# Kernel tuning notes

Measured on AMD Instinct MI355X. Metric: run time of the kernel, lower is better.

The kernel has to match this reference:

```python
import jax, jax.numpy as jnp
import numpy as np

# Topologies derived from init kwargs (inputs=64, outputs=64, state=512, net1 hidden=[512])
D = 64 + 64 + 512                      # 640 = concat(input, prev_output, state)
NET1 = [D, 512, 64]
NET3 = [D] + NET1 + [512]              # [640, 640, 512, 64, 512] (code reuses mutated net1 topo)
W_TOTAL = sum(NET3[j] * NET3[j + 1] for j in range(len(NET3) - 1))  # 802816
B_TOTAL = sum(NET3[1:])                # 1728
NET2 = [D] + NET1 + [W_TOTAL + B_TOTAL]  # [640, 640, 512, 64, 804544]


def _leaky(v):
    return jnp.where(v >= 0, v, 0.01 * v)


def setup_inputs() -> dict:
    key = jax.random.key(0)
    ks = jax.random.split(key, 16)
    inp = {
        "x": jax.random.normal(ks[0], (64,), jnp.float32),
        "prev_output": jnp.zeros((64,), jnp.float32),
        "state": jnp.zeros((512,), jnp.float32),
    }
    # net1 params (Linear stores W as [out, in])
    for i in range(len(NET1) - 1):
        inp[f"net1_w{i}"] = jax.random.normal(ks[1 + i], (NET1[i + 1], NET1[i]), jnp.float32) * 0.02
        inp[f"net1_b{i}"] = jnp.zeros((NET1[i + 1],), jnp.float32)
    # net2 params
    for i in range(len(NET2) - 1):
        inp[f"net2_w{i}"] = jax.random.normal(ks[5 + i], (NET2[i + 1], NET2[i]), jnp.float32) * 0.02
        inp[f"net2_b{i}"] = jnp.zeros((NET2[i + 1],), jnp.float32)
    return inp


def reference(x, prev_output, state,
              net1_w0, net1_b0, net1_w1, net1_b1,
              net2_w0, net2_b0, net2_w1, net2_b1,
              net2_w2, net2_b2, net2_w3, net2_b3):
    inpt = jnp.concatenate([x, prev_output, state])  # [640]

    # net2: hypernetwork producing flattened weights+biases for net3
    h = _leaky(net2_w0 @ inpt + net2_b0)
    h = _leaky(net2_w1 @ h + net2_b1)
    h = _leaky(net2_w2 @ h + net2_b2)
    x2 = jnp.tanh(net2_w3 @ h + net2_b3) * 0.5       # [W_TOTAL + B_TOTAL]
    weights = x2[:W_TOTAL]
    bias = x2[W_TOTAL:]

    # net3: apply generated weights sequentially (state update)
    x3 = inpt
    wi, bi = 0, 0
    for j in range(1, len(NET3)):
        out_d, in_d = NET3[j], NET3[j - 1]
        W = weights[wi:wi + out_d * in_d].reshape(out_d, in_d)
        b = bias[bi:bi + out_d]
        x3 = W @ x3 + b                               # 1D: x3 @ W.T == W @ x3
        if j != len(NET3) - 1:
            x3 = _leaky(x3)
        wi += out_d * in_d
        bi += out_d
    new_state = x3                                    # [512]

    # net1: output head
    h1 = _leaky(net1_w0 @ inpt + net1_b0)
    out = net1_w1 @ h1 + net1_b1                      # [64]

    # torch forward returns only `out`; new_state is the persistent buffer
    # update. We concatenate both so the full step math is observable.
    return jnp.concatenate([out, new_state])          # [576]
```

## Files before the change

### kernel.cpp

```cpp
#include <hip/hip_runtime.h>
#include <math.h>


#define WS_H0    0
#define WS_H1N1  640
#define WS_H1N2  1152
#define WS_H2    1664
#define WS_INPT  1728
#define WS_X3A   2368
#define WS_X3B   3008
#define WS_CNT1  3584
#define WS_CNT2  3585
#define WS_T     4096

#define N_ROWS   804544
#define N_WAVES  12571

__device__ __forceinline__ float leaky_f(float v) { return v >= 0.0f ? v : 0.01f * v; }

__device__ __forceinline__ float inpt_at(int i, const float* x, const float* po, const float* st) {
  return i < 64 ? x[i] : (i < 128 ? po[i - 64] : st[i - 128]);
}

__device__ __forceinline__ float half_tanh(float d) {
  float t = exp2f(d * 2.8853900817779268f);
  return 0.5f - __builtin_amdgcn_rcpf(t + 1.0f);
}

template <int IN>
__device__ __forceinline__ float row_dot(const float* __restrict__ wrow, const float* s_in, int lane) {
  const float4* w4 = (const float4*)wrow;
  const float4* s4 = (const float4*)s_in;
  float acc = 0.f;
  for (int j = lane; j < IN / 4; j += 64) {
    float4 a = w4[j];
    float4 b = s4[j];
    acc += a.x * b.x + a.y * b.y + a.z * b.z + a.w * b.w;
  }
  for (int off = 32; off; off >>= 1) acc += __shfl_xor(acc, off, 64);
  return acc;
}

__global__ __launch_bounds__(256) void k1a(const float* __restrict__ x, const float* __restrict__ po,
                                           const float* __restrict__ st,
                                           const float* __restrict__ w2_0, const float* __restrict__ b2_0,
                                           const float* __restrict__ w1_0, const float* __restrict__ b1_0,
                                           float* __restrict__ ws) {
  if (blockIdx.x == 0 && threadIdx.x < 2) ((int*)ws)[WS_CNT1 + threadIdx.x] = 0;
  __shared__ __align__(16) float s_in[640];
  for (int i = threadIdx.x; i < 640; i += 256) {
    float v = inpt_at(i, x, po, st);
    s_in[i] = v;
    ws[WS_INPT + i] = v;
  }
  __syncthreads();
  int wave = threadIdx.x >> 6, lane = threadIdx.x & 63;
  int o = blockIdx.x * 4 + wave;
  const float* wrow;
  float bias;
  float* dst;
  if (o < 640) {
    wrow = w2_0 + (long long)o * 640; bias = b2_0[o]; dst = ws + WS_H0 + o;
  } else {
    int oo = o - 640;
    wrow = w1_0 + (long long)oo * 640; bias = b1_0[oo]; dst = ws + WS_H1N1 + oo;
  }
  float acc = row_dot<640>(wrow, s_in, lane);
  if (lane == 0) *dst = leaky_f(acc + bias);
}

__global__ __launch_bounds__(256) void k1b(const float* __restrict__ w2_1, const float* __restrict__ b2_1,
                                           const float* __restrict__ w1_1, const float* __restrict__ b1_1,
                                           const float* __restrict__ w2_2, const float* __restrict__ b2_2,
                                           float* __restrict__ ws, float* __restrict__ out) {
  __shared__ __align__(16) float s_h0[640];
  __shared__ __align__(16) float s_h1[512];
  __shared__ int s_last;
  for (int i = threadIdx.x; i < 640; i += 256) s_h0[i] = ws[WS_H0 + i];
  for (int i = threadIdx.x; i < 512; i += 256) s_h1[i] = ws[WS_H1N1 + i];
  __syncthreads();
  int wave = threadIdx.x >> 6, lane = threadIdx.x & 63;
  int o = blockIdx.x * 4 + wave;
  if (o < 512) {
    float acc = row_dot<640>(w2_1 + (long long)o * 640, s_h0, lane);
    if (lane == 0) ws[WS_H1N2 + o] = leaky_f(acc + b2_1[o]);
  } else {
    int oo = o - 512;
    float acc = row_dot<512>(w1_1 + (long long)oo * 512, s_h1, lane);
    if (lane == 0) out[oo] = acc + b1_1[oo];
  }
  __syncthreads();
  __threadfence();
  if (threadIdx.x == 0) s_last = (atomicAdd((int*)ws + WS_CNT1, 1) == (int)gridDim.x - 1);
  __syncthreads();
  if (!s_last) return;
  __threadfence();
  for (int i = threadIdx.x; i < 512; i += 256) s_h1[i] = ws[WS_H1N2 + i];
  __syncthreads();
#pragma unroll
  for (int r = 0; r < 16; r++) {
    int o2 = r * 4 + wave;
    float acc = row_dot<512>(w2_2 + (long long)o2 * 512, s_h1, lane);
    if (lane == 0) ws[WS_H2 + o2] = leaky_f(acc + b2_2[o2]);
  }
}

__global__ __launch_bounds__(256) void bigT(const float* __restrict__ w3, const float* __restrict__ b3,
                                            const float* __restrict__ h2p, float* __restrict__ t) {
  int wid = blockIdx.x * 4 + (threadIdx.x >> 6);
  if (wid >= N_WAVES) return;
  const int lane = threadIdx.x & 63;
  const int g = lane >> 4;
  const int gl = lane & 15;
  float4 hv = ((const float4*)h2p)[gl];
  const long long base = (long long)wid * 64;
  const int myrow = (gl << 2) + g;
  float bmine = b3[base + myrow];
  const float4* wp = (const float4*)(w3 + (base << 6));
  float4 v[16];
#pragma unroll
  for (int q = 0; q < 16; q++) v[q] = wp[((q * 4 + g) << 4) + gl];
  float myd = 0.f;
#pragma unroll
  for (int q = 0; q < 16; q++) {
    float d = v[q].x * hv.x + v[q].y * hv.y + v[q].z * hv.z + v[q].w * hv.w;
    d += __shfl_xor(d, 1, 64);
    d += __shfl_xor(d, 2, 64);
    d += __shfl_xor(d, 4, 64);
    d += __shfl_xor(d, 8, 64);
    if (gl == q) myd = d;
  }
  t[base + myrow] = half_tanh(myd + bmine);
}

template <int IN, bool LEAKY>
__global__ __launch_bounds__(256) void gml(const float* __restrict__ t, const float* __restrict__ x3in,
                                           float* __restrict__ x3out, long long wi, long long brow,
                                           int OUT) {
  __shared__ __align__(16) float s_in[IN];
  for (int i = threadIdx.x; i < IN; i += 256) s_in[i] = x3in[i];
  __syncthreads();
  int wave = threadIdx.x >> 6, lane = threadIdx.x & 63;
  int o = blockIdx.x * 4 + wave;
  if (o >= OUT) return;
  float acc = row_dot<IN>(t + wi + (long long)o * IN, s_in, lane);
  if (lane == 0) {
    acc += t[brow + o];
    x3out[o] = LEAKY ? leaky_f(acc) : acc;
  }
}

__global__ __launch_bounds__(1024) void gml2Tail(const float* __restrict__ t, float* __restrict__ ws,
                                                 float* __restrict__ out) {
  __shared__ __align__(16) float s_in[640];
  __shared__ __align__(16) float s_c[64];
  __shared__ int s_last;
  const int tid = threadIdx.x;
  const int wave = tid >> 6, lane = tid & 63;
  for (int i = tid; i < 640; i += 1024) s_in[i] = ws[WS_X3A + i];
  __syncthreads();
  {
    int o = blockIdx.x * 16 + wave;
    float acc = row_dot<640>(t + 409600 + (long long)o * 640, s_in, lane);
    if (lane == 0) ws[WS_X3B + o] = leaky_f(acc + t[803456 + o]);
  }
  __syncthreads();
  __threadfence();
  if (tid == 0) s_last = (atomicAdd((int*)ws + WS_CNT2, 1) == (int)gridDim.x - 1);
  __syncthreads();
  if (!s_last) return;
  __threadfence();
  for (int i = tid; i < 512; i += 1024) s_in[i] = ws[WS_X3B + i];
  __syncthreads();
#pragma unroll
  for (int r = 0; r < 4; r++) {
    int o3 = wave + r * 16;
    float acc = row_dot<512>(t + 737280 + (long long)o3 * 512, s_in, lane);
    if (lane == 0) s_c[o3] = leaky_f(acc + t[803968 + o3]);
  }
  __syncthreads();
  const int g = lane >> 4, glx = lane & 15;
  float4 xc4 = ((const float4*)s_c)[glx];
#pragma unroll
  for (int r = 0; r < 8; r++) {
    int o4 = r * 64 + wave * 4 + g;
    const float4* row = (const float4*)(t + 770048 + (long long)o4 * 64);
    float4 wv = row[glx];
    float a = wv.x * xc4.x + wv.y * xc4.y + wv.z * xc4.z + wv.w * xc4.w;
    a += __shfl_xor(a, 1, 64);
    a += __shfl_xor(a, 2, 64);
    a += __shfl_xor(a, 4, 64);
    a += __shfl_xor(a, 8, 64);
    if (glx == 0) out[64 + o4] = a + t[804032 + o4];
  }
}

extern "C" void kernel_launch(void* const* d_in, const int* in_sizes, int n_in,
                              void* d_out, int out_size, void* d_ws, size_t ws_size,
                              hipStream_t stream) {
  const float* x    = (const float*)d_in[0];
  const float* po   = (const float*)d_in[1];
  const float* st   = (const float*)d_in[2];
  const float* w1_0 = (const float*)d_in[3];
  const float* b1_0 = (const float*)d_in[4];
  const float* w1_1 = (const float*)d_in[5];
  const float* b1_1 = (const float*)d_in[6];
  const float* w2_0 = (const float*)d_in[7];
  const float* b2_0 = (const float*)d_in[8];
  const float* w2_1 = (const float*)d_in[9];
  const float* b2_1 = (const float*)d_in[10];
  const float* w2_2 = (const float*)d_in[11];
  const float* b2_2 = (const float*)d_in[12];
  const float* w3   = (const float*)d_in[13];
  const float* b3   = (const float*)d_in[14];
  float* ws  = (float*)d_ws;
  float* out = (float*)d_out;
  float* t   = ws + WS_T;

  k1a<<<288, 256, 0, stream>>>(x, po, st, w2_0, b2_0, w1_0, b1_0, ws);
  k1b<<<144, 256, 0, stream>>>(w2_1, b2_1, w1_1, b1_1, w2_2, b2_2, ws, out);
  bigT<<<(N_WAVES + 3) / 4, 256, 0, stream>>>(w3, b3, ws + WS_H2, t);
  gml<640, true><<<160, 256, 0, stream>>>(t, ws + WS_INPT, ws + WS_X3A, 0LL, 802816LL, 640);
  gml2Tail<<<32, 1024, 0, stream>>>(t, ws, out);
}
```

Measured before the change: 378.9 us.

## Fuse first generated layer into bigT via partial sums and last-block reduction

```diff
diff --git a/kernel.cpp b/kernel.cpp
--- a/kernel.cpp
+++ b/kernel.cpp
@@ -11,10 +11,14 @@
 #define WS_X3B   3008
 #define WS_CNT1  3584
 #define WS_CNT2  3585
+#define WS_CNT3  3586
 #define WS_T     4096
+#define WS_PART  808640
 
 #define N_ROWS   804544
 #define N_WAVES  12571
+
+typedef float vf4 __attribute__((ext_vector_type(4)));
 
 __device__ __forceinline__ float leaky_f(float v) { return v >= 0.0f ? v : 0.01f * v; }
 
@@ -46,7 +50,7 @@
                                            const float* __restrict__ w2_0, const float* __restrict__ b2_0,
                                            const float* __restrict__ w1_0, const float* __restrict__ b1_0,
                                            float* __restrict__ ws) {
-  if (blockIdx.x == 0 && threadIdx.x < 2) ((int*)ws)[WS_CNT1 + threadIdx.x] = 0;
+  if (blockIdx.x == 0 && threadIdx.x < 3) ((int*)ws)[WS_CNT1 + threadIdx.x] = 0;
   __shared__ __align__(16) float s_in[640];
   for (int i = threadIdx.x; i < 640; i += 256) {
     float v = inpt_at(i, x, po, st);
@@ -69,10 +73,10 @@
   if (lane == 0) *dst = leaky_f(acc + bias);
 }
 
-__global__ __launch_bounds__(256) void k1b(const float* __restrict__ w2_1, const float* __restrict__ b2_1,
-                                           const float* __restrict__ w1_1, const float* __restrict__ b1_1,
-                                           const float* __restrict__ w2_2, const float* __restrict__ b2_2,
-                                           float* __restrict__ ws, float* __restrict__ out) {
+__global__ __launch_bounds__(256) void k1bc(const float* __restrict__ w2_1, const float* __restrict__ b2_1,
+                                            const float* __restrict__ w1_1, const float* __restrict__ b1_1,
+                                            const float* __restrict__ w2_2, const float* __restrict__ b2_2,
+                                            float* __restrict__ ws, float* __restrict__ out) {
   __shared__ __align__(16) float s_h0[640];
   __shared__ __align__(16) float s_h1[512];
   __shared__ int s_last;
@@ -106,20 +110,23 @@
 }
 
 __global__ __launch_bounds__(256) void bigT(const float* __restrict__ w3, const float* __restrict__ b3,
-                                            const float* __restrict__ h2p, float* __restrict__ t) {
+                                            float* __restrict__ ws) {
+  float* t = ws + WS_T;
+  __shared__ int s_last;
   int wid = blockIdx.x * 4 + (threadIdx.x >> 6);
-  if (wid >= N_WAVES) return;
+  const bool active = wid < N_WAVES;
+  if (!active) wid = 0;
   const int lane = threadIdx.x & 63;
   const int g = lane >> 4;
   const int gl = lane & 15;
-  float4 hv = ((const float4*)h2p)[gl];
+  float4 hv = ((const float4*)(ws + WS_H2))[gl];
   const long long base = (long long)wid * 64;
   const int myrow = (gl << 2) + g;
   float bmine = b3[base + myrow];
-  const float4* wp = (const float4*)(w3 + (base << 6));
-  float4 v[16];
-#pragma unroll
-  for (int q = 0; q < 16; q++) v[q] = wp[((q * 4 + g) << 4) + gl];
+  const vf4* wp = (const vf4*)(w3 + (base << 6));
+  vf4 v[16];
+#pragma unroll
+  for (int q = 0; q < 16; q++) v[q] = __builtin_nontemporal_load(&wp[((q * 4 + g) << 4) + gl]);
   float myd = 0.f;
 #pragma unroll
   for (int q = 0; q < 16; q++) {
@@ -130,37 +137,45 @@
     d += __shfl_xor(d, 8, 64);
     if (gl == q) myd = d;
   }
-  t[base + myrow] = half_tanh(myd + bmine);
-}
-
-template <int IN, bool LEAKY>
-__global__ __launch_bounds__(256) void gml(const float* __restrict__ t, const float* __restrict__ x3in,
-                                           float* __restrict__ x3out, long long wi, long long brow,
-                                           int OUT) {
-  __shared__ __align__(16) float s_in[IN];
-  for (int i = threadIdx.x; i < IN; i += 256) s_in[i] = x3in[i];
-  __syncthreads();
-  int wave = threadIdx.x >> 6, lane = threadIdx.x & 63;
-  int o = blockIdx.x * 4 + wave;
-  if (o >= OUT) return;
-  float acc = row_dot<IN>(t + wi + (long long)o * IN, s_in, lane);
-  if (lane == 0) {
-    acc += t[brow + o];
-    x3out[o] = LEAKY ? leaky_f(acc) : acc;
-  }
-}
-
-__global__ __launch_bounds__(1024) void gml2Tail(const float* __restrict__ t, float* __restrict__ ws,
-                                                 float* __restrict__ out) {
+  float tval = half_tanh(myd + bmine);
+  if (active) t[base + myrow] = tval;
+  if (active && wid < 6400) {
+    int o = wid / 10, chunk = wid - o * 10;
+    float p = tval * ws[WS_INPT + chunk * 64 + myrow];
+    p += __shfl_xor(p, 1, 64);
+    p += __shfl_xor(p, 2, 64);
+    p += __shfl_xor(p, 4, 64);
+    p += __shfl_xor(p, 8, 64);
+    p += __shfl_xor(p, 16, 64);
+    p += __shfl_xor(p, 32, 64);
+    if (lane == 0) ws[WS_PART + o * 10 + chunk] = p;
+  }
+  __syncthreads();
+  __threadfence();
+  if (threadIdx.x == 0) s_last = (atomicAdd((int*)ws + WS_CNT3, 1) == (int)gridDim.x - 1);
+  __syncthreads();
+  if (!s_last) return;
+  __threadfence();
+  for (int o = threadIdx.x; o < 640; o += 256) {
+    const float* pp = ws + WS_PART + o * 10;
+    float s = 0.f;
+#pragma unroll
+    for (int c = 0; c < 10; c++) s += pp[c];
+    ws[WS_X3A + o] = leaky_f(s + t[802816 + o]);
+  }
+}
+
+__global__ __launch_bounds__(256) void gml2tail(const float* __restrict__ t, float* __restrict__ ws,
+                                                float* __restrict__ out) {
   __shared__ __align__(16) float s_in[640];
   __shared__ __align__(16) float s_c[64];
   __shared__ int s_last;
   const int tid = threadIdx.x;
   const int wave = tid >> 6, lane = tid & 63;
-  for (int i = tid; i < 640; i += 1024) s_in[i] = ws[WS_X3A + i];
+  for (int i = tid; i < 640; i += 256) s_in[i] = ws[WS_X3A + i];
   __syncthreads();
   {
-    int o = blockIdx.x * 16 + wave;
+    int o = blockIdx.x * 4 + wave;
     float acc = row_dot<640>(t + 409600 + (long long)o * 640, s_in, lane);
     if (lane == 0) ws[WS_X3B + o] = leaky_f(acc + t[803456 + o]);
   }
@@ -170,11 +185,11 @@
   __syncthreads();
   if (!s_last) return;
   __threadfence();
-  for (int i = tid; i < 512; i += 1024) s_in[i] = ws[WS_X3B + i];
-  __syncthreads();
-#pragma unroll
-  for (int r = 0; r < 4; r++) {
-    int o3 = wave + r * 16;
+  for (int i = tid; i < 512; i += 256) s_in[i] = ws[WS_X3B + i];
+  __syncthreads();
+#pragma unroll
+  for (int r = 0; r < 16; r++) {
+    int o3 = r * 4 + wave;
     float acc = row_dot<512>(t + 737280 + (long long)o3 * 512, s_in, lane);
     if (lane == 0) s_c[o3] = leaky_f(acc + t[803968 + o3]);
   }
@@ -182,8 +197,8 @@
   const int g = lane >> 4, glx = lane & 15;
   float4 xc4 = ((const float4*)s_c)[glx];
 #pragma unroll
-  for (int r = 0; r < 8; r++) {
-    int o4 = r * 64 + wave * 4 + g;
+  for (int r = 0; r < 32; r++) {
+    int o4 = r * 16 + wave * 4 + g;
     const float4* row = (const float4*)(t + 770048 + (long long)o4 * 64);
     float4 wv = row[glx];
     float a = wv.x * xc4.x + wv.y * xc4.y + wv.z * xc4.z + wv.w * xc4.w;
@@ -218,8 +233,7 @@
   float* t   = ws + WS_T;
 
   k1a<<<288, 256, 0, stream>>>(x, po, st, w2_0, b2_0, w1_0, b1_0, ws);
-  k1b<<<144, 256, 0, stream>>>(w2_1, b2_1, w1_1, b1_1, w2_2, b2_2, ws, out);
-  bigT<<<(N_WAVES + 3) / 4, 256, 0, stream>>>(w3, b3, ws + WS_H2, t);
-  gml<640, true><<<160, 256, 0, stream>>>(t, ws + WS_INPT, ws + WS_X3A, 0LL, 802816LL, 640);
-  gml2Tail<<<32, 1024, 0, stream>>>(t, ws, out);
-}
+  k1bc<<<144, 256, 0, stream>>>(w2_1, b2_1, w1_1, b1_1, w2_2, b2_2, ws, out);
+  bigT<<<(N_WAVES + 3) / 4, 256, 0, stream>>>(w3, b3, ws);
+  gml2tail<<<128, 256, 0, stream>>>(t, ws, out);
+}
```

New measurement: 920.6 us. +143.0%, slower.
